# Optimization experiments

Measured on AMD Instinct MI355X. Metric: run time of the kernel, lower is better.

## Reference

```python
import jax, jax.numpy as jnp
import numpy as np

HID = 1024
VOCAB = 50257
MAXLEN = 2048


def setup_inputs() -> dict:
    key = jax.random.key(0)
    ks = jax.random.split(key, 12)
    s = 0.02
    return {
        "input_tok": jax.random.randint(ks[0], (1,), 0, VOCAB),
        "hidden": jax.random.normal(ks[1], (1, 1, HID), jnp.float32),
        "encoder_outputs": jax.random.normal(ks[2], (MAXLEN, HID), jnp.float32),
        "emb": jax.random.normal(ks[3], (VOCAB, HID), jnp.float32) * s,
        "attn_W": jax.random.normal(ks[4], (MAXLEN, 2 * HID), jnp.float32) * s,
        "attn_b": jnp.zeros((MAXLEN,), jnp.float32),
        "comb_W": jax.random.normal(ks[5], (HID, 2 * HID), jnp.float32) * s,
        "comb_b": jnp.zeros((HID,), jnp.float32),
        "W_ih": jax.random.normal(ks[6], (3 * HID, HID), jnp.float32) * s,
        "W_hh": jax.random.normal(ks[7], (3 * HID, HID), jnp.float32) * s,
        "b_ih": jnp.zeros((3 * HID,), jnp.float32),
        "b_hh": jnp.zeros((3 * HID,), jnp.float32),
        "out_W": jax.random.normal(ks[8], (VOCAB, HID), jnp.float32) * s,
        "out_b": jnp.zeros((VOCAB,), jnp.float32),
    }


def reference(input_tok, hidden, encoder_outputs, emb, attn_W, attn_b,
              comb_W, comb_b, W_ih, W_hh, b_ih, b_hh, out_W, out_b):
    H = hidden.shape[-1]
    # embedding lookup -> [1, H]; dropout is identity in eval mode
    embedded = emb[input_tok].reshape(1, H)
    h = hidden[0]  # [1, H]
    # Bahdanau-style attention over fixed max_length
    attn_weights = jax.nn.softmax(
        jnp.concatenate([embedded, h], axis=1) @ attn_W.T + attn_b, axis=1)  # [1, L]
    attn_applied = attn_weights @ encoder_outputs  # [1, H]
    x = jnp.concatenate([embedded, attn_applied], axis=1) @ comb_W.T + comb_b
    x = jax.nn.relu(x)  # [1, H]
    # single GRU step (PyTorch gate layout: r, z, n)
    gi = x @ W_ih.T + b_ih
    gh = h @ W_hh.T + b_hh
    gi_r, gi_z, gi_n = jnp.split(gi, 3, axis=1)
    gh_r, gh_z, gh_n = jnp.split(gh, 3, axis=1)
    r = jax.nn.sigmoid(gi_r + gh_r)
    z = jax.nn.sigmoid(gi_z + gh_z)
    n = jnp.tanh(gi_n + r * gh_n)
    h_new = (1.0 - z) * n + z * h  # [1, H]
    out = jax.nn.log_softmax(h_new @ out_W.T + out_b, axis=1)  # [1, V]
    return out, h_new[None], attn_weights
```

## Files before the change

### kernel.cpp

```cpp
#include <hip/hip_runtime.h>
#include <math.h>

#define HID    1024
#define VOCAB  50257
#define MAXLEN 2048
#define LOGIT_BLOCKS ((VOCAB + 3) / 4)

#define WS_SCORES    0
#define WS_ATTNW     2048
#define WS_APPLIED   4096
#define WS_X         5120
#define WS_GI        6144
#define WS_GH        9216
#define WS_HNEW      12288
#define WS_MAXCELL   13312
#define WS_LSE       13313
#define WS_SUMPART   13440
#define WS_PARTIALS  16384

__device__ inline float wave_reduce_sum(float v) {
    #pragma unroll
    for (int m = 32; m > 0; m >>= 1) v += __shfl_xor(v, m, 64);
    return v;
}

__global__ void k_attn_scores(const float* __restrict__ emb, const int* __restrict__ tok,
                              const float* __restrict__ hidden,
                              const float* __restrict__ attn_W, const float* __restrict__ attn_b,
                              float* __restrict__ scores) {
    int gtid = blockIdx.x * blockDim.x + threadIdx.x;
    int row = gtid >> 6, lane = gtid & 63;
    if (row >= MAXLEN) return;
    const float* erow = emb + (size_t)tok[0] * HID;
    const float* wrow = attn_W + (size_t)row * (2 * HID);
    float acc = 0.f;
    #pragma unroll
    for (int i = 0; i < 8; ++i) {
        int k = i * 256 + lane * 4;
        float4 w = *(const float4*)(wrow + k);
        float4 c = (k < HID) ? *(const float4*)(erow + k)
                             : *(const float4*)(hidden + (k - HID));
        acc += w.x * c.x + w.y * c.y + w.z * c.z + w.w * c.w;
    }
    acc = wave_reduce_sum(acc);
    if (lane == 0) scores[row] = acc + attn_b[row];
}

__global__ __launch_bounds__(1024) void k_softmax2048(const float* __restrict__ scores,
                                                      float* __restrict__ out_w,
                                                      float* __restrict__ ws_w) {
    __shared__ float sm[1024];
    int t = threadIdx.x;
    float s0 = scores[t], s1 = scores[t + 1024];
    sm[t] = fmaxf(s0, s1);
    __syncthreads();
    for (int s = 512; s > 0; s >>= 1) { if (t < s) sm[t] = fmaxf(sm[t], sm[t + s]); __syncthreads(); }
    float m = sm[0];
    __syncthreads();
    float e0 = expf(s0 - m), e1 = expf(s1 - m);
    sm[t] = e0 + e1;
    __syncthreads();
    for (int s = 512; s > 0; s >>= 1) { if (t < s) sm[t] += sm[t + s]; __syncthreads(); }
    float inv = 1.f / sm[0];
    out_w[t] = e0 * inv; out_w[t + 1024] = e1 * inv;
    ws_w[t]  = e0 * inv; ws_w[t + 1024]  = e1 * inv;
}

__global__ void k_attn_apply_partial(const float* __restrict__ E, const float* __restrict__ w,
                                     float* __restrict__ partials) {
    int b = blockIdx.x, t = threadIdx.x;
    int j = t * 4;
    float4 acc = make_float4(0.f, 0.f, 0.f, 0.f);
    int r0 = b * 32;
    for (int r = 0; r < 32; ++r) {
        float wr = w[r0 + r];
        float4 e = *(const float4*)(E + (size_t)(r0 + r) * HID + j);
        acc.x += wr * e.x; acc.y += wr * e.y; acc.z += wr * e.z; acc.w += wr * e.w;
    }
    *(float4*)(partials + (size_t)b * HID + j) = acc;
}

__global__ void k_attn_apply_reduce(const float* __restrict__ partials, float* __restrict__ applied) {
    int j = blockIdx.x * blockDim.x + threadIdx.x;
    float acc = 0.f;
    for (int c = 0; c < 64; ++c) acc += partials[c * HID + j];
    applied[j] = acc;
}

__global__ void k_comb(const float* __restrict__ emb, const int* __restrict__ tok,
                       const float* __restrict__ applied,
                       const float* __restrict__ comb_W, const float* __restrict__ comb_b,
                       float* __restrict__ x) {
    int gtid = blockIdx.x * blockDim.x + threadIdx.x;
    int row = gtid >> 6, lane = gtid & 63;
    if (row >= HID) return;
    const float* erow = emb + (size_t)tok[0] * HID;
    const float* wrow = comb_W + (size_t)row * (2 * HID);
    float acc = 0.f;
    #pragma unroll
    for (int i = 0; i < 8; ++i) {
        int k = i * 256 + lane * 4;
        float4 w = *(const float4*)(wrow + k);
        float4 c = (k < HID) ? *(const float4*)(erow + k)
                             : *(const float4*)(applied + (k - HID));
        acc += w.x * c.x + w.y * c.y + w.z * c.z + w.w * c.w;
    }
    acc = wave_reduce_sum(acc);
    if (lane == 0) x[row] = fmaxf(acc + comb_b[row], 0.f);
}

__global__ void k_gru_gemv(const float* __restrict__ W_ih, const float* __restrict__ W_hh,
                           const float* __restrict__ b_ih, const float* __restrict__ b_hh,
                           const float* __restrict__ x, const float* __restrict__ h,
                           float* __restrict__ gi, float* __restrict__ gh) {
    int gtid = blockIdx.x * blockDim.x + threadIdx.x;
    int row = gtid >> 6, lane = gtid & 63;
    if (row >= 6 * HID) return;
    const float* wrow; const float* vec;
    if (row < 3 * HID) { wrow = W_ih + (size_t)row * HID; vec = x; }
    else               { wrow = W_hh + (size_t)(row - 3 * HID) * HID; vec = h; }
    float acc = 0.f;
    #pragma unroll
    for (int i = 0; i < 4; ++i) {
        int k = i * 256 + lane * 4;
        float4 w = *(const float4*)(wrow + k);
        float4 c = *(const float4*)(vec + k);
        acc += w.x * c.x + w.y * c.y + w.z * c.z + w.w * c.w;
    }
    acc = wave_reduce_sum(acc);
    if (lane == 0) {
        if (row < 3 * HID) gi[row] = acc + b_ih[row];
        else               gh[row - 3 * HID] = acc + b_hh[row - 3 * HID];
    }
}

__global__ void k_gru_gate(const float* __restrict__ gi, const float* __restrict__ gh,
                           const float* __restrict__ h,
                           float* __restrict__ hnew_out, float* __restrict__ hnew_ws) {
    int i = blockIdx.x * blockDim.x + threadIdx.x;
    float r = 1.f / (1.f + expf(-(gi[i] + gh[i])));
    float z = 1.f / (1.f + expf(-(gi[i + HID] + gh[i + HID])));
    float n = tanhf(gi[i + 2 * HID] + r * gh[i + 2 * HID]);
    float hn = (1.f - z) * n + z * h[i];
    hnew_out[i] = hn;
    hnew_ws[i]  = hn;
}

__global__ void k_logits(const float* __restrict__ hnew, const float* __restrict__ out_W,
                         const float* __restrict__ out_b,
                         float* __restrict__ logits, float* __restrict__ blockmax) {
    __shared__ float wmax[4];
    int wib = threadIdx.x >> 6, lane = threadIdx.x & 63;
    int row = blockIdx.x * 4 + wib;
    float acc = 0.f;
    if (row < VOCAB) {
        const float* wrow = out_W + (size_t)row * HID;
        #pragma unroll
        for (int i = 0; i < 4; ++i) {
            int k = i * 256 + lane * 4;
            float4 w = *(const float4*)(wrow + k);
            float4 c = *(const float4*)(hnew + k);
            acc += w.x * c.x + w.y * c.y + w.z * c.z + w.w * c.w;
        }
        acc = wave_reduce_sum(acc);
        if (lane == 0) { acc += out_b[row]; logits[row] = acc; }
    }
    if (lane == 0) wmax[wib] = (row < VOCAB) ? acc : -INFINITY;
    __syncthreads();
    if (threadIdx.x == 0)
        blockmax[blockIdx.x] = fmaxf(fmaxf(wmax[0], wmax[1]), fmaxf(wmax[2], wmax[3]));
}

__global__ __launch_bounds__(1024) void k_maxreduce(const float* __restrict__ blockmax,
                                                    float* __restrict__ maxcell) {
    __shared__ float sm[1024];
    int t = threadIdx.x;
    float m = -INFINITY;
    for (int i = t; i < LOGIT_BLOCKS; i += 1024) m = fmaxf(m, blockmax[i]);
    sm[t] = m;
    __syncthreads();
    for (int s = 512; s > 0; s >>= 1) { if (t < s) sm[t] = fmaxf(sm[t], sm[t + s]); __syncthreads(); }
    if (t == 0) maxcell[0] = sm[0];
}

__global__ void k_sumexp(const float* __restrict__ logits, const float* __restrict__ maxcell,
                         float* __restrict__ partials) {
    __shared__ float sm[4];
    float m = maxcell[0];
    float acc = 0.f;
    for (int v = blockIdx.x * blockDim.x + threadIdx.x; v < VOCAB; v += gridDim.x * blockDim.x)
        acc += expf(logits[v] - m);
    acc = wave_reduce_sum(acc);
    int wib = threadIdx.x >> 6, lane = threadIdx.x & 63;
    if (lane == 0) sm[wib] = acc;
    __syncthreads();
    if (threadIdx.x == 0) partials[blockIdx.x] = sm[0] + sm[1] + sm[2] + sm[3];
}

__global__ void k_finalize(const float* __restrict__ partials, const float* __restrict__ maxcell,
                           float* __restrict__ lse) {
    __shared__ float a[2];
    float v = partials[threadIdx.x];
    v = wave_reduce_sum(v);
    if ((threadIdx.x & 63) == 0) a[threadIdx.x >> 6] = v;
    __syncthreads();
    if (threadIdx.x == 0) lse[0] = maxcell[0] + logf(a[0] + a[1]);
}

__global__ void k_writeout(float* __restrict__ out, const float* __restrict__ lse) {
    int v = blockIdx.x * blockDim.x + threadIdx.x;
    if (v < VOCAB) out[v] -= lse[0];
}

extern "C" void kernel_launch(void* const* d_in, const int* in_sizes, int n_in,
                              void* d_out, int out_size, void* d_ws, size_t ws_size,
                              hipStream_t stream) {
    const int*   tok     = (const int*)d_in[0];
    const float* hidden  = (const float*)d_in[1];
    const float* E       = (const float*)d_in[2];
    const float* emb     = (const float*)d_in[3];
    const float* attn_W  = (const float*)d_in[4];
    const float* attn_b  = (const float*)d_in[5];
    const float* comb_W  = (const float*)d_in[6];
    const float* comb_b  = (const float*)d_in[7];
    const float* W_ih    = (const float*)d_in[8];
    const float* W_hh    = (const float*)d_in[9];
    const float* b_ih    = (const float*)d_in[10];
    const float* b_hh    = (const float*)d_in[11];
    const float* out_W   = (const float*)d_in[12];
    const float* out_b   = (const float*)d_in[13];

    float* out       = (float*)d_out;
    float* hnew_out  = out + VOCAB;
    float* attnw_out = out + VOCAB + HID;

    float* ws        = (float*)d_ws;
    float* scores    = ws + WS_SCORES;
    float* attnw_ws  = ws + WS_ATTNW;
    float* applied   = ws + WS_APPLIED;
    float* x         = ws + WS_X;
    float* gi        = ws + WS_GI;
    float* gh        = ws + WS_GH;
    float* hnew_ws   = ws + WS_HNEW;
    float* maxcell   = ws + WS_MAXCELL;
    float* lse       = ws + WS_LSE;
    float* sumpart   = ws + WS_SUMPART;
    float* partials  = ws + WS_PARTIALS;
    float* blockmax  = ws + WS_PARTIALS;

    k_attn_scores<<<MAXLEN / 4, 256, 0, stream>>>(emb, tok, hidden, attn_W, attn_b, scores);
    k_softmax2048<<<1, 1024, 0, stream>>>(scores, attnw_out, attnw_ws);
    k_attn_apply_partial<<<64, 256, 0, stream>>>(E, attnw_ws, partials);
    k_attn_apply_reduce<<<4, 256, 0, stream>>>(partials, applied);
    k_comb<<<HID / 4, 256, 0, stream>>>(emb, tok, applied, comb_W, comb_b, x);
    k_gru_gemv<<<(6 * HID) / 4, 256, 0, stream>>>(W_ih, W_hh, b_ih, b_hh, x, hidden, gi, gh);
    k_gru_gate<<<HID / 256, 256, 0, stream>>>(gi, gh, hidden, hnew_out, hnew_ws);
    k_logits<<<LOGIT_BLOCKS, 256, 0, stream>>>(hnew_ws, out_W, out_b, out, blockmax);
    k_maxreduce<<<1, 1024, 0, stream>>>(blockmax, maxcell);
    k_sumexp<<<128, 256, 0, stream>>>(out, maxcell, sumpart);
    k_finalize<<<1, 128, 0, stream>>>(sumpart, maxcell, lse);
    k_writeout<<<(VOCAB + 255) / 256, 256, 0, stream>>>(out, lse);
}
```

Measured before the change: 73.46 us.

## Fuse attention softmax into apply and use online log-sum-exp for logits

Each of 128 blocks now recomputes the attention softmax statistics redundantly and directly applies its slice of weights to encoder outputs, removing the standalone single-block softmax kernel. The logits kernel emits per-block max and scaled exp-sum, so one finalize kernel computes the log-sum-exp with an online rescale, replacing the separate max, sumexp, and finalize kernels. This cuts kernel launches and a second pass over the logits. The cost is redundant per-block softmax work and a wider 128-way partial reduction.

```diff
diff --git a/kernel.cpp b/kernel.cpp
--- a/kernel.cpp
+++ b/kernel.cpp
@@ -5,18 +5,19 @@
 #define VOCAB  50257
 #define MAXLEN 2048
 #define LOGIT_BLOCKS ((VOCAB + 3) / 4)
+#define SMB 128
+#define SMR (MAXLEN / SMB)
 
 #define WS_SCORES    0
-#define WS_ATTNW     2048
 #define WS_APPLIED   4096
 #define WS_X         5120
 #define WS_GI        6144
 #define WS_GH        9216
 #define WS_HNEW      12288
-#define WS_MAXCELL   13312
 #define WS_LSE       13313
-#define WS_SUMPART   13440
-#define WS_PARTIALS  16384
+#define WS_PM        16384
+#define WS_PS        30720
+#define WS_PARTIALS  49152
 
 __device__ inline float wave_reduce_sum(float v) {
     #pragma unroll
@@ -24,10 +25,11 @@
     return v;
 }
 
-__global__ void k_attn_scores(const float* __restrict__ emb, const int* __restrict__ tok,
-                              const float* __restrict__ hidden,
-                              const float* __restrict__ attn_W, const float* __restrict__ attn_b,
-                              float* __restrict__ scores) {
+__global__ __launch_bounds__(256) void k_attn_scores(
+        const float* __restrict__ emb, const int* __restrict__ tok,
+        const float* __restrict__ hidden,
+        const float* __restrict__ attn_W, const float* __restrict__ attn_b,
+        float* __restrict__ scores) {
     int gtid = blockIdx.x * blockDim.x + threadIdx.x;
     int row = gtid >> 6, lane = gtid & 63;
     if (row >= MAXLEN) return;
@@ -46,51 +48,55 @@
     if (lane == 0) scores[row] = acc + attn_b[row];
 }
 
-__global__ __launch_bounds__(1024) void k_softmax2048(const float* __restrict__ scores,
-                                                      float* __restrict__ out_w,
-                                                      float* __restrict__ ws_w) {
-    __shared__ float sm[1024];
-    int t = threadIdx.x;
-    float s0 = scores[t], s1 = scores[t + 1024];
-    sm[t] = fmaxf(s0, s1);
+__global__ __launch_bounds__(256) void k_softmax_apply(
+        const float* __restrict__ scores, const float* __restrict__ E,
+        float* __restrict__ out_w, float* __restrict__ partials) {
+    __shared__ float red[256];
+    __shared__ float wrow[SMR];
+    int t = threadIdx.x, b = blockIdx.x;
+    float v[8];
+    float m = -INFINITY;
+    #pragma unroll
+    for (int i = 0; i < 8; ++i) { v[i] = scores[t + 256 * i]; m = fmaxf(m, v[i]); }
+    red[t] = m; __syncthreads();
+    for (int s = 128; s > 0; s >>= 1) { if (t < s) red[t] = fmaxf(red[t], red[t + s]); __syncthreads(); }
+    float M = red[0]; __syncthreads();
+    float s = 0.f;
+    #pragma unroll
+    for (int i = 0; i < 8; ++i) s += expf(v[i] - M);
+    red[t] = s; __syncthreads();
+    for (int k = 128; k > 0; k >>= 1) { if (t < k) red[t] += red[t + k]; __syncthreads(); }
+    float invS = 1.f / red[0];
+    int r0 = b * SMR;
+    if (t < SMR) wrow[t] = expf(scores[r0 + t] - M) * invS;
     __syncthreads();
-    for (int s = 512; s > 0; s >>= 1) { if (t < s) sm[t] = fmaxf(sm[t], sm[t + s]); __syncthreads(); }
-    float m = sm[0];
-    __syncthreads();
-    float e0 = expf(s0 - m), e1 = expf(s1 - m);
-    sm[t] = e0 + e1;
-    __syncthreads();
-    for (int s = 512; s > 0; s >>= 1) { if (t < s) sm[t] += sm[t + s]; __syncthreads(); }
-    float inv = 1.f / sm[0];
-    out_w[t] = e0 * inv; out_w[t + 1024] = e1 * inv;
-    ws_w[t]  = e0 * inv; ws_w[t + 1024]  = e1 * inv;
-}
-
-__global__ void k_attn_apply_partial(const float* __restrict__ E, const float* __restrict__ w,
-                                     float* __restrict__ partials) {
-    int b = blockIdx.x, t = threadIdx.x;
     int j = t * 4;
     float4 acc = make_float4(0.f, 0.f, 0.f, 0.f);
-    int r0 = b * 32;
-    for (int r = 0; r < 32; ++r) {
-        float wr = w[r0 + r];
+    for (int r = 0; r < SMR; ++r) {
+        float w = wrow[r];
         float4 e = *(const float4*)(E + (size_t)(r0 + r) * HID + j);
-        acc.x += wr * e.x; acc.y += wr * e.y; acc.z += wr * e.z; acc.w += wr * e.w;
+        acc.x += w * e.x; acc.y += w * e.y; acc.z += w * e.z; acc.w += w * e.w;
     }
     *(float4*)(partials + (size_t)b * HID + j) = acc;
-}
-
-__global__ void k_attn_apply_reduce(const float* __restrict__ partials, float* __restrict__ applied) {
+    if (b == 0) {
+        #pragma unroll
+        for (int i = 0; i < 8; ++i) out_w[t + 256 * i] = expf(v[i] - M) * invS;
+    }
+}
+
+__global__ __launch_bounds__(256) void k_apply_reduce(
+        const float* __restrict__ partials, float* __restrict__ applied) {
     int j = blockIdx.x * blockDim.x + threadIdx.x;
     float acc = 0.f;
-    for (int c = 0; c < 64; ++c) acc += partials[c * HID + j];
+    for (int c = 0; c < SMB; ++c) acc += partials[(size_t)c * HID + j];
     applied[j] = acc;
 }
 
-__global__ void k_comb(const float* __restrict__ emb, const int* __restrict__ tok,
-                       const float* __restrict__ applied,
-                       const float* __restrict__ comb_W, const float* __restrict__ comb_b,
-                       float* __restrict__ x) {
+__global__ __launch_bounds__(256) void k_comb(
+        const float* __restrict__ emb, const int* __restrict__ tok,
+        const float* __restrict__ applied,
+        const float* __restrict__ comb_W, const float* __restrict__ comb_b,
+        float* __restrict__ x) {
     int gtid = blockIdx.x * blockDim.x + threadIdx.x;
     int row = gtid >> 6, lane = gtid & 63;
     if (row >= HID) return;
@@ -109,10 +115,11 @@
     if (lane == 0) x[row] = fmaxf(acc + comb_b[row], 0.f);
 }
 
-__global__ void k_gru_gemv(const float* __restrict__ W_ih, const float* __restrict__ W_hh,
-                           const float* __restrict__ b_ih, const float* __restrict__ b_hh,
-                           const float* __restrict__ x, const float* __restrict__ h,
-                           float* __restrict__ gi, float* __restrict__ gh) {
+__global__ __launch_bounds__(256) void k_gru_gemv(
+        const float* __restrict__ W_ih, const float* __restrict__ W_hh,
+        const float* __restrict__ b_ih, const float* __restrict__ b_hh,
+        const float* __restrict__ x, const float* __restrict__ h,
+        float* __restrict__ gi, float* __restrict__ gh) {
     int gtid = blockIdx.x * blockDim.x + threadIdx.x;
     int row = gtid >> 6, lane = gtid & 63;
     if (row >= 6 * HID) return;
@@ -134,9 +141,10 @@
     }
 }
 
-__global__ void k_gru_gate(const float* __restrict__ gi, const float* __restrict__ gh,
-                           const float* __restrict__ h,
-                           float* __restrict__ hnew_out, float* __restrict__ hnew_ws) {
+__global__ __launch_bounds__(256) void k_gru_gate(
+        const float* __restrict__ gi, const float* __restrict__ gh,
+        const float* __restrict__ h,
+        float* __restrict__ hnew_out, float* __restrict__ hnew_ws) {
     int i = blockIdx.x * blockDim.x + threadIdx.x;
     float r = 1.f / (1.f + expf(-(gi[i] + gh[i])));
     float z = 1.f / (1.f + expf(-(gi[i + HID] + gh[i + HID])));
@@ -146,10 +154,11 @@
     hnew_ws[i]  = hn;
 }
 
-__global__ void k_logits(const float* __restrict__ hnew, const float* __restrict__ out_W,
-                         const float* __restrict__ out_b,
-                         float* __restrict__ logits, float* __restrict__ blockmax) {
-    __shared__ float wmax[4];
+__global__ __launch_bounds__(256) void k_logits(
+        const float* __restrict__ hnew, const float* __restrict__ out_W,
+        const float* __restrict__ out_b,
+        float* __restrict__ logits, float* __restrict__ pm, float* __restrict__ ps) {
+    __shared__ float wl[4];
     int wib = threadIdx.x >> 6, lane = threadIdx.x & 63;
     int row = blockIdx.x * 4 + wib;
     float acc = 0.f;
@@ -165,49 +174,35 @@
         acc = wave_reduce_sum(acc);
         if (lane == 0) { acc += out_b[row]; logits[row] = acc; }
     }
-    if (lane == 0) wmax[wib] = (row < VOCAB) ? acc : -INFINITY;
+    if (lane == 0) wl[wib] = (row < VOCAB) ? acc : -INFINITY;
     __syncthreads();
-    if (threadIdx.x == 0)
-        blockmax[blockIdx.x] = fmaxf(fmaxf(wmax[0], wmax[1]), fmaxf(wmax[2], wmax[3]));
-}
-
-__global__ __launch_bounds__(1024) void k_maxreduce(const float* __restrict__ blockmax,
-                                                    float* __restrict__ maxcell) {
-    __shared__ float sm[1024];
+    if (threadIdx.x == 0) {
+        float m = fmaxf(fmaxf(wl[0], wl[1]), fmaxf(wl[2], wl[3]));
+        float s = expf(wl[0] - m) + expf(wl[1] - m) + expf(wl[2] - m) + expf(wl[3] - m);
+        pm[blockIdx.x] = m;
+        ps[blockIdx.x] = s;
+    }
+}
+
+__global__ __launch_bounds__(1024) void k_lse_finalize(
+        const float* __restrict__ pm, const float* __restrict__ ps,
+        float* __restrict__ lse) {
+    __shared__ float red[1024];
     int t = threadIdx.x;
     float m = -INFINITY;
-    for (int i = t; i < LOGIT_BLOCKS; i += 1024) m = fmaxf(m, blockmax[i]);
-    sm[t] = m;
-    __syncthreads();
-    for (int s = 512; s > 0; s >>= 1) { if (t < s) sm[t] = fmaxf(sm[t], sm[t + s]); __syncthreads(); }
-    if (t == 0) maxcell[0] = sm[0];
-}
-
-__global__ void k_sumexp(const float* __restrict__ logits, const float* __restrict__ maxcell,
-                         float* __restrict__ partials) {
-    __shared__ float sm[4];
-    float m = maxcell[0];
-    float acc = 0.f;
-    for (int v = blockIdx.x * blockDim.x + threadIdx.x; v < VOCAB; v += gridDim.x * blockDim.x)
-        acc += expf(logits[v] - m);
-    acc = wave_reduce_sum(acc);
-    int wib = threadIdx.x >> 6, lane = threadIdx.x & 63;
-    if (lane == 0) sm[wib] = acc;
-    __syncthreads();
-    if (threadIdx.x == 0) partials[blockIdx.x] = sm[0] + sm[1] + sm[2] + sm[3];
-}
-
-__global__ void k_finalize(const float* __restrict__ partials, const float* __restrict__ maxcell,
-                           float* __restrict__ lse) {
-    __shared__ float a[2];
-    float v = partials[threadIdx.x];
-    v = wave_reduce_sum(v);
-    if ((threadIdx.x & 63) == 0) a[threadIdx.x >> 6] = v;
-    __syncthreads();
-    if (threadIdx.x == 0) lse[0] = maxcell[0] + logf(a[0] + a[1]);
-}
-
-__global__ void k_writeout(float* __restrict__ out, const float* __restrict__ lse) {
+    for (int i = t; i < LOGIT_BLOCKS; i += 1024) m = fmaxf(m, pm[i]);
+    red[t] = m; __syncthreads();
+    for (int s = 512; s > 0; s >>= 1) { if (t < s) red[t] = fmaxf(red[t], red[t + s]); __syncthreads(); }
+    float M = red[0]; __syncthreads();
+    float acc = 0.f;
+    for (int i = t; i < LOGIT_BLOCKS; i += 1024) acc += ps[i] * expf(pm[i] - M);
+    red[t] = acc; __syncthreads();
+    for (int s = 512; s > 0; s >>= 1) { if (t < s) red[t] += red[t + s]; __syncthreads(); }
+    if (t == 0) lse[0] = M + logf(red[0]);
+}
+
+__global__ __launch_bounds__(256) void k_writeout(float* __restrict__ out,
+                                                  const float* __restrict__ lse) {
     int v = blockIdx.x * blockDim.x + threadIdx.x;
     if (v < VOCAB) out[v] -= lse[0];
 }
@@ -236,28 +231,23 @@
 
     float* ws        = (float*)d_ws;
     float* scores    = ws + WS_SCORES;
-    float* attnw_ws  = ws + WS_ATTNW;
     float* applied   = ws + WS_APPLIED;
     float* x         = ws + WS_X;
     float* gi        = ws + WS_GI;
     float* gh        = ws + WS_GH;
     float* hnew_ws   = ws + WS_HNEW;
-    float* maxcell   = ws + WS_MAXCELL;
     float* lse       = ws + WS_LSE;
-    float* sumpart   = ws + WS_SUMPART;
+    float* pm        = ws + WS_PM;
+    float* ps        = ws + WS_PS;
     float* partials  = ws + WS_PARTIALS;
-    float* blockmax  = ws + WS_PARTIALS;
 
     k_attn_scores<<<MAXLEN / 4, 256, 0, stream>>>(emb, tok, hidden, attn_W, attn_b, scores);
-    k_softmax2048<<<1, 1024, 0, stream>>>(scores, attnw_out, attnw_ws);
-    k_attn_apply_partial<<<64, 256, 0, stream>>>(E, attnw_ws, partials);
-    k_attn_apply_reduce<<<4, 256, 0, stream>>>(partials, applied);
+    k_softmax_apply<<<SMB, 256, 0, stream>>>(scores, E, attnw_out, partials);
+    k_apply_reduce<<<HID / 256, 256, 0, stream>>>(partials, applied);
     k_comb<<<HID / 4, 256, 0, stream>>>(emb, tok, applied, comb_W, comb_b, x);
     k_gru_gemv<<<(6 * HID) / 4, 256, 0, stream>>>(W_ih, W_hh, b_ih, b_hh, x, hidden, gi, gh);
     k_gru_gate<<<HID / 256, 256, 0, stream>>>(gi, gh, hidden, hnew_out, hnew_ws);
-    k_logits<<<LOGIT_BLOCKS, 256, 0, stream>>>(hnew_ws, out_W, out_b, out, blockmax);
-    k_maxreduce<<<1, 1024, 0, stream>>>(blockmax, maxcell);
-    k_sumexp<<<128, 256, 0, stream>>>(out, maxcell, sumpart);
-    k_finalize<<<1, 128, 0, stream>>>(sumpart, maxcell, lse);
+    k_logits<<<LOGIT_BLOCKS, 256, 0, stream>>>(hnew_ws, out_W, out_b, out, pm, ps);
+    k_lse_finalize<<<1, 1024, 0, stream>>>(pm, ps, lse);
     k_writeout<<<(VOCAB + 255) / 256, 256, 0, stream>>>(out, lse);
 }
```

Result: no change. 74.25 us (+1.1%).
